# Performance work log

Hardware: AMD Instinct MI355X
Metric: run time of the kernel (lower is better)

Reference implementation:

```python
import jax, jax.numpy as jnp
import numpy as np
import math

N = 40000
E = 1280000
HID = 128
NF = 128
NG = 50
L = 3
CUTOFF = 10.0


def ssp(x):
    # shifted softplus: softplus(x) - log(2)
    return jax.nn.softplus(x) - jnp.float32(math.log(2.0))


def setup_inputs() -> dict:
    key = jax.random.key(0)
    ks = jax.random.split(key, 16)
    z = jax.random.randint(ks[0], (N,), 0, 100)
    pos = jax.random.normal(ks[1], (N, 3), dtype=jnp.float32) * 3.0
    batch = jnp.zeros((N,), dtype=jnp.int32)
    edge_index = jax.random.randint(ks[2], (2, E), 0, N)
    s = 0.1
    emb = jax.random.normal(ks[3], (100, HID), dtype=jnp.float32) * s
    mlp_w1 = jax.random.normal(ks[4], (L, NG, NF), dtype=jnp.float32) * s
    mlp_b1 = jnp.zeros((L, NF), dtype=jnp.float32)
    mlp_w2 = jax.random.normal(ks[5], (L, NF, NF), dtype=jnp.float32) * s
    mlp_b2 = jnp.zeros((L, NF), dtype=jnp.float32)
    conv_w1 = jax.random.normal(ks[6], (L, HID, NF), dtype=jnp.float32) * s  # no bias
    conv_w2 = jax.random.normal(ks[7], (L, NF, HID), dtype=jnp.float32) * s
    conv_b2 = jnp.zeros((L, HID), dtype=jnp.float32)
    lin_w = jax.random.normal(ks[8], (L, HID, HID), dtype=jnp.float32) * s
    lin_b = jnp.zeros((L, HID), dtype=jnp.float32)
    lin1_w = jax.random.normal(ks[9], (HID, HID // 2), dtype=jnp.float32) * s
    lin1_b = jnp.zeros((HID // 2,), dtype=jnp.float32)
    return {
        "z": z, "pos": pos, "batch": batch, "edge_index": edge_index,
        "emb": emb, "mlp_w1": mlp_w1, "mlp_b1": mlp_b1, "mlp_w2": mlp_w2,
        "mlp_b2": mlp_b2, "conv_w1": conv_w1, "conv_w2": conv_w2,
        "conv_b2": conv_b2, "lin_w": lin_w, "lin_b": lin_b,
        "lin1_w": lin1_w, "lin1_b": lin1_b,
    }


def reference(z, pos, batch, edge_index, emb, mlp_w1, mlp_b1, mlp_w2, mlp_b2,
              conv_w1, conv_w2, conv_b2, lin_w, lin_b, lin1_w, lin1_b):
    n = z.shape[0]
    row, col = edge_index[0], edge_index[1]
    # edge distances (radius-graph edge weights)
    diff = pos[row] - pos[col]                       # [E,3]
    edge_weight = jnp.sqrt(jnp.sum(diff * diff, axis=-1))  # [E]
    # Gaussian smearing
    offset = jnp.linspace(0.0, CUTOFF, NG, dtype=jnp.float32)
    coeff = -0.5 / (offset[1] - offset[0]) ** 2
    edge_attr = jnp.exp(coeff * (edge_weight[:, None] - offset[None, :]) ** 2)  # [E,NG]
    # cosine cutoff
    C = 0.5 * (jnp.cos(edge_weight * (jnp.pi / CUTOFF)) + 1.0)  # [E]

    h = emb[z]  # [N,HID]
    for l in range(L):
        W = ssp(edge_attr @ mlp_w1[l] + mlp_b1[l]) @ mlp_w2[l] + mlp_b2[l]  # [E,NF]
        W = W * C[:, None]
        x = h @ conv_w1[l]                      # [N,NF]
        msg = x[row] * W                        # gather + filter, [E,NF]
        agg = jax.ops.segment_sum(msg, col, num_segments=n)  # scatter-add, [N,NF]
        x = agg @ conv_w2[l] + conv_b2[l]       # [N,HID]
        x = ssp(x)
        x = x @ lin_w[l] + lin_b[l]
        h = h + x
    return ssp(h @ lin1_w + lin1_b)  # [N,HID//2]
```

## Files before the change

### kernel.cpp

```cpp
#include <hip/hip_runtime.h>
#include <math.h>


typedef _Float16 f16;
typedef _Float16 half8 __attribute__((ext_vector_type(8)));
typedef _Float16 half4v __attribute__((ext_vector_type(4)));
typedef float f32x4 __attribute__((ext_vector_type(4)));

#define NGAUSS 50
#define HIDF   128
#define NBINS  8192
#define DMAXF  40.0f
#define NLAYER 3
#define XST    132
#define BSHIFT 9
#define MAXBUCK 128
#define SCAP  20480

static __device__ __forceinline__ float sspf(float v) {
    return fmaxf(v, 0.0f) + log1pf(expf(-fabsf(v))) - 0.6931471805599453f;
}

__global__ __launch_bounds__(256) void k_stage(const int* __restrict__ ei,
                                               const float* __restrict__ pos,
                                               int* __restrict__ scnt,
                                               uint2* __restrict__ staging,
                                               int E, int nbuck) {
    const float SCALE = (float)(NBINS - 1) / DMAXF;
    __shared__ int bhist[MAXBUCK];
    __shared__ int boff[MAXBUCK];
    __shared__ int gpos[MAXBUCK];
    __shared__ uint2 recs[4096];
    __shared__ unsigned char lbuck[4096];
    int t = threadIdx.x;
    for (int i = t; i < nbuck; i += 256) bhist[i] = 0;
    __syncthreads();
    int e0 = blockIdx.x * 4096;
    int cnt_here = min(4096, E - e0);
    unsigned pay[16];
    unsigned short cc[16];
    short rk[16];
#pragma unroll
    for (int k = 0; k < 16; ++k) {
        int idx = t + k * 256;
        rk[k] = -1;
        if (idx < cnt_here) {
            int e = e0 + idx;
            int r = ei[e], c = ei[E + e];
            float dx = pos[3*r+0] - pos[3*c+0];
            float dy = pos[3*r+1] - pos[3*c+1];
            float dz = pos[3*r+2] - pos[3*c+2];
            float d = sqrtf(dx*dx + dy*dy + dz*dz);
            float u = fminf(d * SCALE, (float)(NBINS - 1));
            int i0 = min((int)u, NBINS - 2);
            float w0 = u - (float)i0;
            int wq = (int)(w0 * 8.0f + 0.5f);
            if (wq == 8) { i0 = min(i0 + 1, NBINS - 2); wq = 0; }
            pay[k] = ((unsigned)i0 << 19) | ((unsigned)wq << 16) | (unsigned)r;
            cc[k] = (unsigned short)c;
            rk[k] = (short)atomicAdd(&bhist[c >> BSHIFT], 1);
        }
    }
    __syncthreads();
    if (t == 0) {
        int run = 0;
        for (int b = 0; b < nbuck; ++b) { boff[b] = run; run += bhist[b]; }
    }
    __syncthreads();
    if (t < nbuck) gpos[t] = atomicAdd(&scnt[t], bhist[t]);
    __syncthreads();
#pragma unroll
    for (int k = 0; k < 16; ++k) {
        if (rk[k] >= 0) {
            int b = cc[k] >> BSHIFT;
            int slot = boff[b] + rk[k];
            recs[slot] = make_uint2(pay[k], (unsigned)cc[k]);
            lbuck[slot] = (unsigned char)b;
        }
    }
    __syncthreads();
    for (int i = t; i < cnt_here; i += 256) {
        int b = lbuck[i];
        staging[(size_t)b * SCAP + gpos[b] + (i - boff[b])] = recs[i];
    }
}

__global__ __launch_bounds__(1024) void k_place(const uint2* __restrict__ staging,
                                                const int* __restrict__ scnt,
                                                int* __restrict__ meta,
                                                int* __restrict__ offs,
                                                int n, int nbuck) {
    __shared__ int lcnt[512], loff[512], lcur[512];
    __shared__ int ldsm[SCAP];
    __shared__ int ebase_s;
    int b = blockIdx.x, t = threadIdx.x;
    int cntb = scnt[b];
    if (t == 0) {
        int run = 0;
        for (int j = 0; j < b; ++j) run += scnt[j];
        ebase_s = run;
    }
    for (int j = t; j < 512; j += 1024) { lcnt[j] = 0; lcur[j] = 0; }
    __syncthreads();
    int ebase = ebase_s;
    const uint2* sb = staging + (size_t)b * SCAP;
    for (int i = t; i < cntb; i += 1024)
        atomicAdd(&lcnt[sb[i].y & 511], 1);
    __syncthreads();
    if (t < 512) loff[t] = lcnt[t];
    __syncthreads();
    for (int o = 1; o < 512; o <<= 1) {
        int v = 0;
        if (t < 512) { v = loff[t]; if (t >= o) v += loff[t - o]; }
        __syncthreads();
        if (t < 512) loff[t] = v;
        __syncthreads();
    }
    int nb0 = b << BSHIFT;
    if (t < 512) {
        int node = nb0 + t;
        if (node < n) offs[node] = ebase + loff[t] - lcnt[t];
    }
    if (b == nbuck - 1 && t == 0) offs[n] = ebase + cntb;
    __syncthreads();
    for (int i = t; i < cntb; i += 1024) {
        uint2 r = sb[i];
        int cl = (int)(r.y & 511);
        int lpos = (loff[cl] - lcnt[cl]) + atomicAdd(&lcur[cl], 1);
        if (lpos < SCAP) ldsm[lpos] = (int)r.x;
        else meta[ebase + lpos] = (int)r.x;
    }
    __syncthreads();
    int lim = min(cntb, SCAP);
    for (int i = t; i < lim; i += 1024) meta[ebase + i] = ldsm[i];
}

__global__ __launch_bounds__(128) void k_table(const float* __restrict__ w1,
                                               const float* __restrict__ b1,
                                               const float* __restrict__ w2,
                                               const float* __restrict__ b2,
                                               f16* __restrict__ T) {
    const float DELTA = 10.0f / 49.0f;
    const float COEFF = -0.5f / (DELTA * DELTA);
    const float HSTEP = DMAXF / (float)(NBINS - 1);
    __shared__ float ea[8][NGAUSS];
    __shared__ float u[8][HIDF];
    int l = blockIdx.y, b0 = blockIdx.x * 8, j = threadIdx.x;
    for (int idx = j; idx < 8 * NGAUSS; idx += 128) {
        int bb = idx / NGAUSS, g = idx % NGAUSS;
        float d = (float)(b0 + bb) * HSTEP;
        float diff = d - (float)g * DELTA;
        ea[bb][g] = expf(COEFF * diff * diff);
    }
    __syncthreads();
    float acc[8];
    {
        float bias = b1[l * HIDF + j];
#pragma unroll
        for (int b = 0; b < 8; ++b) acc[b] = bias;
        const float* w1l = w1 + (size_t)l * NGAUSS * HIDF;
        for (int g = 0; g < NGAUSS; ++g) {
            float wv = w1l[g * HIDF + j];
#pragma unroll
            for (int b = 0; b < 8; ++b) acc[b] = fmaf(ea[b][g], wv, acc[b]);
        }
#pragma unroll
        for (int b = 0; b < 8; ++b) u[b][j] = sspf(acc[b]);
    }
    __syncthreads();
    {
        float bias = b2[l * HIDF + j];
#pragma unroll
        for (int b = 0; b < 8; ++b) acc[b] = bias;
        const float* w2l = w2 + (size_t)l * HIDF * HIDF;
        for (int k = 0; k < HIDF; ++k) {
            float wv = w2l[k * HIDF + j];
#pragma unroll
            for (int b = 0; b < 8; ++b) acc[b] = fmaf(u[b][k], wv, acc[b]);
        }
    }
    f16* Tl = T + ((size_t)l * NBINS + b0) * HIDF;
#pragma unroll
    for (int b = 0; b < 8; ++b) {
        float d = (float)(b0 + b) * HSTEP;
        float C = 0.5f * (cosf(d * (float)(M_PI / 10.0)) + 1.0f);
        Tl[b * HIDF + j] = (f16)(acc[b] * C);
    }
}

__global__ void k_wpack(const float* __restrict__ cw1, const float* __restrict__ cw2,
                        const float* __restrict__ lw, const float* __restrict__ l1w,
                        f16* __restrict__ Wp) {
    int mat = blockIdx.y;
    int N = (mat == 9) ? 64 : HIDF;
    int ntiles = N >> 4;
    int tid = blockIdx.x * 256 + threadIdx.x;
    int lane = tid & 63, ks = (tid >> 6) & 3, nt = tid >> 8;
    if (nt >= ntiles) return;
    const float* W;
    if (mat < 9) {
        int l = mat / 3, kind = mat % 3;
        W = (kind == 0 ? cw1 : kind == 1 ? cw2 : lw) + (size_t)l * HIDF * HIDF;
    } else {
        W = l1w;
    }
    int kbase = ks * 32 + (lane >> 4) * 8;
    int col = nt * 16 + (lane & 15);
    half8 st;
#pragma unroll
    for (int j = 0; j < 8; ++j) st[j] = (f16)W[(size_t)(kbase + j) * N + col];
    *(half8*)&Wp[(size_t)mat * 16384 + ((size_t)(nt * 4 + ks) * 64 + lane) * 8] = st;
}

#define AGG_EDGE(yy)                                                         \
    {                                                                        \
        int row_ = (yy) & 0xFFFF;                                            \
        int i0_ = ((unsigned)(yy)) >> 19;                                    \
        float w0_ = (float)(((yy) >> 16) & 7) * 0.125f;                      \
        half8 x0_ = *(const half8*)&xj[(size_t)row_ * HIDF];                 \
        half8 ta_ = *(const half8*)&Tj[(size_t)i0_ * HIDF];                  \
        half8 tb_ = *(const half8*)&Tj[(size_t)(i0_ + 1) * HIDF];            \
        _Pragma("unroll")                                                    \
        for (int j = 0; j < 8; ++j) {                                        \
            float t0 = (float)ta_[j];                                        \
            float f0 = fmaf(w0_, (float)tb_[j] - t0, t0);                    \
            a[j] = fmaf((float)x0_[j], f0, a[j]);                            \
        }                                                                    \
    }

__global__ __launch_bounds__(256) void k_agg(const f16* __restrict__ x,
                                             const f16* __restrict__ T,
                                             const int* __restrict__ meta,
                                             const int* __restrict__ offs,
                                             f16* __restrict__ agg, int n) {
    int node = (blockIdx.x * blockDim.x + threadIdx.x) >> 4;
    int lane = threadIdx.x & 15;
    if (node >= n) return;
    int beg = offs[node], end = offs[node + 1];
    const f16* xj = x + lane * 8;
    const f16* Tj = T + lane * 8;
    float a[8] = {};
    for (int chunk = beg; chunk < end; chunk += 16) {
        int cnt = min(16, end - chunk);
        int mm = meta[chunk + min(lane, cnt - 1)];
        int q = 0;
        for (; q + 4 <= cnt; q += 4) {
            int y0 = __shfl(mm, q + 0, 16);
            int y1 = __shfl(mm, q + 1, 16);
            int y2 = __shfl(mm, q + 2, 16);
            int y3 = __shfl(mm, q + 3, 16);
            AGG_EDGE(y0)
            AGG_EDGE(y1)
            AGG_EDGE(y2)
            AGG_EDGE(y3)
        }
        for (; q < cnt; ++q) {
            int y0 = __shfl(mm, q, 16);
            AGG_EDGE(y0)
        }
    }
    half8 st;
#pragma unroll
    for (int j = 0; j < 8; ++j) st[j] = (f16)a[j];
    *(half8*)&agg[(size_t)node * HIDF + lane * 8] = st;
}

__global__ __launch_bounds__(256) void k_init_gemm(const int* __restrict__ z,
                                                   const float* __restrict__ emb,
                                                   const f16* __restrict__ w1p,
                                                   f16* __restrict__ xout) {
    int lane = threadIdx.x & 63;
    int wid = threadIdx.x >> 6;
    int m0 = blockIdx.x * 64 + wid * 16;
    int mrow = lane & 15, quad = lane >> 4;
    const float* er = emb + (size_t)z[m0 + mrow] * HIDF + quad * 8;
    half8 afr[4];
#pragma unroll
    for (int ks = 0; ks < 4; ++ks) {
        float4 a = *(const float4*)(er + ks * 32);
        float4 b = *(const float4*)(er + ks * 32 + 4);
        half8 f = {(f16)a.x, (f16)a.y, (f16)a.z, (f16)a.w,
                   (f16)b.x, (f16)b.y, (f16)b.z, (f16)b.w};
        afr[ks] = f;
    }
    f32x4 acc[8];
#pragma unroll
    for (int t = 0; t < 8; ++t) acc[t] = (f32x4){0.f, 0.f, 0.f, 0.f};
    const f16* bp = w1p + (size_t)lane * 8;
#pragma unroll
    for (int t = 0; t < 8; ++t)
#pragma unroll
        for (int ks = 0; ks < 4; ++ks) {
            half8 bfr = *(const half8*)(bp + (size_t)(t * 4 + ks) * 512);
            acc[t] = __builtin_amdgcn_mfma_f32_16x16x32_f16(afr[ks], bfr, acc[t], 0, 0, 0);
        }
    int col0 = lane & 15;
    int growb = m0 + quad * 4;
#pragma unroll
    for (int t = 0; t < 8; ++t)
#pragma unroll
        for (int r = 0; r < 4; ++r)
            xout[(size_t)(growb + r) * HIDF + t * 16 + col0] = (f16)acc[t][r];
}

template <int NT3, bool LAYER0, bool WRITE_H>
__global__ __launch_bounds__(256) void k_fused(const f16* __restrict__ agg,
                                               const f16* __restrict__ w2p,
                                               const float* __restrict__ b2,
                                               const f16* __restrict__ lwp,
                                               const float* __restrict__ lb,
                                               const f16* __restrict__ b3p,
                                               const float* __restrict__ b3,
                                               float* __restrict__ hio,
                                               const int* __restrict__ z,
                                               const float* __restrict__ emb,
                                               f16* __restrict__ xout,
                                               float* __restrict__ fout) {
    __shared__ f16 Xs[4][16][XST];
    int lane = threadIdx.x & 63;
    int wid = threadIdx.x >> 6;
    int m0 = blockIdx.x * 64 + wid * 16;
    int mrow = lane & 15, quad = lane >> 4;
    int col0 = mrow;
    int growb = m0 + quad * 4;
    f16 (*X)[XST] = Xs[wid];

    half8 afr[4];
    {
        const f16* Ar = agg + (size_t)(m0 + mrow) * HIDF + quad * 8;
#pragma unroll
        for (int ks = 0; ks < 4; ++ks) afr[ks] = *(const half8*)(Ar + ks * 32);
    }
    f32x4 acc[8];
#pragma unroll
    for (int t = 0; t < 8; ++t) acc[t] = (f32x4){0.f, 0.f, 0.f, 0.f};
    {
        const f16* bp = w2p + (size_t)lane * 8;
#pragma unroll
        for (int t = 0; t < 8; ++t)
#pragma unroll
            for (int ks = 0; ks < 4; ++ks) {
                half8 bfr = *(const half8*)(bp + (size_t)(t * 4 + ks) * 512);
                acc[t] = __builtin_amdgcn_mfma_f32_16x16x32_f16(afr[ks], bfr, acc[t], 0, 0, 0);
            }
    }
#pragma unroll
    for (int t = 0; t < 8; ++t) {
        int col = t * 16 + col0;
        float bv = b2[col];
#pragma unroll
        for (int r = 0; r < 4; ++r)
            X[quad * 4 + r][col] = (f16)sspf(acc[t][r] + bv);
    }
#pragma unroll
    for (int ks = 0; ks < 4; ++ks) {
        half4v lo = *(const half4v*)&X[mrow][ks * 32 + quad * 8];
        half4v hi = *(const half4v*)&X[mrow][ks * 32 + quad * 8 + 4];
        half8 f;
#pragma unroll
        for (int j = 0; j < 4; ++j) { f[j] = lo[j]; f[4 + j] = hi[j]; }
        afr[ks] = f;
    }
#pragma unroll
    for (int t = 0; t < 8; ++t) acc[t] = (f32x4){0.f, 0.f, 0.f, 0.f};
    {
        const f16* bp = lwp + (size_t)lane * 8;
#pragma unroll
        for (int t = 0; t < 8; ++t)
#pragma unroll
            for (int ks = 0; ks < 4; ++ks) {
                half8 bfr = *(const half8*)(bp + (size_t)(t * 4 + ks) * 512);
                acc[t] = __builtin_amdgcn_mfma_f32_16x16x32_f16(afr[ks], bfr, acc[t], 0, 0, 0);
            }
    }
    int zr[4];
    if (LAYER0) {
#pragma unroll
        for (int r = 0; r < 4; ++r) zr[r] = z[growb + r];
    }
#pragma unroll
    for (int t = 0; t < 8; ++t) {
        int col = t * 16 + col0;
        float bv = lb[col];
#pragma unroll
        for (int r = 0; r < 4; ++r) {
            int grow = growb + r;
            float resid = LAYER0 ? emb[(size_t)zr[r] * HIDF + col]
                                 : hio[(size_t)grow * HIDF + col];
            float hp = acc[t][r] + bv + resid;
            if (WRITE_H) hio[(size_t)grow * HIDF + col] = hp;
            X[quad * 4 + r][col] = (f16)hp;
        }
    }
#pragma unroll
    for (int ks = 0; ks < 4; ++ks) {
        half4v lo = *(const half4v*)&X[mrow][ks * 32 + quad * 8];
        half4v hi = *(const half4v*)&X[mrow][ks * 32 + quad * 8 + 4];
        half8 f;
#pragma unroll
        for (int j = 0; j < 4; ++j) { f[j] = lo[j]; f[4 + j] = hi[j]; }
        afr[ks] = f;
    }
#pragma unroll
    for (int t = 0; t < NT3; ++t) acc[t] = (f32x4){0.f, 0.f, 0.f, 0.f};
    {
        const f16* bp = b3p + (size_t)lane * 8;
#pragma unroll
        for (int t = 0; t < NT3; ++t)
#pragma unroll
            for (int ks = 0; ks < 4; ++ks) {
                half8 bfr = *(const half8*)(bp + (size_t)(t * 4 + ks) * 512);
                acc[t] = __builtin_amdgcn_mfma_f32_16x16x32_f16(afr[ks], bfr, acc[t], 0, 0, 0);
            }
    }
    if (NT3 == 8) {
#pragma unroll
        for (int t = 0; t < 8; ++t)
#pragma unroll
            for (int r = 0; r < 4; ++r)
                xout[(size_t)(growb + r) * HIDF + t * 16 + col0] = (f16)acc[t][r];
    } else {
#pragma unroll
        for (int t = 0; t < NT3; ++t) {
            int col = t * 16 + col0;
            float bv = b3[col];
#pragma unroll
            for (int r = 0; r < 4; ++r)
                fout[(size_t)(growb + r) * (NT3 * 16) + col] = sspf(acc[t][r] + bv);
        }
    }
}

extern "C" void kernel_launch(void* const* d_in, const int* in_sizes, int n_in,
                              void* d_out, int out_size, void* d_ws, size_t ws_size,
                              hipStream_t stream) {
    const int*   z       = (const int*)d_in[0];
    const float* pos     = (const float*)d_in[1];
    const int*   ei      = (const int*)d_in[3];
    const float* emb     = (const float*)d_in[4];
    const float* mlp_w1  = (const float*)d_in[5];
    const float* mlp_b1  = (const float*)d_in[6];
    const float* mlp_w2  = (const float*)d_in[7];
    const float* mlp_b2  = (const float*)d_in[8];
    const float* conv_w1 = (const float*)d_in[9];
    const float* conv_w2 = (const float*)d_in[10];
    const float* conv_b2 = (const float*)d_in[11];
    const float* lin_w   = (const float*)d_in[12];
    const float* lin_b   = (const float*)d_in[13];
    const float* lin1_w  = (const float*)d_in[14];
    const float* lin1_b  = (const float*)d_in[15];
    float* out = (float*)d_out;

    int n = in_sizes[0];
    int E = in_sizes[3] / 2;
    int nbuck = (n + 511) >> 9;

    char* ws = (char*)d_ws;
    size_t off = 0;
    auto alloc = [&](size_t bytes) -> void* {
        void* p = ws + off;
        off = (off + bytes + 255) & ~(size_t)255;
        return p;
    };
    float* h     = (float*)alloc((size_t)n * HIDF * 4);
    f16*   x16   = (f16*)alloc((size_t)n * HIDF * 2);
    f16*   agg16 = (f16*)alloc((size_t)n * HIDF * 2);
    f16*   T16   = (f16*)alloc((size_t)NLAYER * NBINS * HIDF * 2);
    int*   meta  = (int*)alloc((size_t)E * 4);
    int*   offs  = (int*)alloc((size_t)(n + 1) * 4);
    int*   scnt  = (int*)alloc((size_t)nbuck * 4);
    uint2* staging = (uint2*)alloc((size_t)nbuck * SCAP * 8);
    f16*   Wp    = (f16*)alloc((size_t)10 * 16384 * 2);

    const int tb = 256;
    hipMemsetAsync(scnt, 0, (size_t)nbuck * 4, stream);
    hipLaunchKernelGGL(k_stage, dim3((E + 4095) / 4096), dim3(tb), 0, stream,
                       ei, pos, scnt, staging, E, nbuck);
    hipLaunchKernelGGL(k_place, dim3(nbuck), dim3(1024), 0, stream,
                       staging, scnt, meta, offs, n, nbuck);
    hipLaunchKernelGGL(k_wpack, dim3(8, 10), dim3(tb), 0, stream,
                       conv_w1, conv_w2, lin_w, lin1_w, Wp);
    hipLaunchKernelGGL(k_table, dim3(NBINS / 8, NLAYER), dim3(128), 0, stream,
                       mlp_w1, mlp_b1, mlp_w2, mlp_b2, T16);

    int gemmblocks = n / 64;
    int aggblocks = (n * 16 + tb - 1) / tb;
    hipLaunchKernelGGL(k_init_gemm, dim3(gemmblocks), dim3(tb), 0, stream,
                       z, emb, Wp + (size_t)0 * 16384, x16);
    hipLaunchKernelGGL(k_agg, dim3(aggblocks), dim3(tb), 0, stream,
                       x16, T16 + (size_t)0 * NBINS * HIDF, meta, offs, agg16, n);
    hipLaunchKernelGGL(HIP_KERNEL_NAME(k_fused<8, true, true>), dim3(gemmblocks), dim3(tb), 0, stream,
                       agg16, Wp + (size_t)1 * 16384, conv_b2 + 0 * HIDF,
                       Wp + (size_t)2 * 16384, lin_b + 0 * HIDF,
                       Wp + (size_t)3 * 16384, (const float*)nullptr,
                       h, z, emb, x16, (float*)nullptr);
    hipLaunchKernelGGL(k_agg, dim3(aggblocks), dim3(tb), 0, stream,
                       x16, T16 + (size_t)1 * NBINS * HIDF, meta, offs, agg16, n);
    hipLaunchKernelGGL(HIP_KERNEL_NAME(k_fused<8, false, true>), dim3(gemmblocks), dim3(tb), 0, stream,
                       agg16, Wp + (size_t)4 * 16384, conv_b2 + 1 * HIDF,
                       Wp + (size_t)5 * 16384, lin_b + 1 * HIDF,
                       Wp + (size_t)6 * 16384, (const float*)nullptr,
                       h, (const int*)nullptr, (const float*)nullptr, x16, (float*)nullptr);
    hipLaunchKernelGGL(k_agg, dim3(aggblocks), dim3(tb), 0, stream,
                       x16, T16 + (size_t)2 * NBINS * HIDF, meta, offs, agg16, n);
    hipLaunchKernelGGL(HIP_KERNEL_NAME(k_fused<4, false, false>), dim3(gemmblocks), dim3(tb), 0, stream,
                       agg16, Wp + (size_t)7 * 16384, conv_b2 + 2 * HIDF,
                       Wp + (size_t)8 * 16384, lin_b + 2 * HIDF,
                       Wp + (size_t)9 * 16384, lin1_b,
                       h, (const int*)nullptr, (const float*)nullptr, (f16*)nullptr, out);
    (void)n_in; (void)out_size; (void)ws_size;
}
```

Baseline: 436.8 us.

## Expand filter table to 64K bins and use nearest-bin lookup in aggregation

The coarse 8192-bin filter table is expanded by a new kernel into a fine 65536-bin table via linear interpolation, so each edge stores a single rounded bin index instead of a bin plus quantized weight. The aggregation loop drops the second table load and the interpolation math per edge, and is unrolled to issue eight edges' loads before the FMAs. The fine table is 48 MB across three layers, which may raise cache pressure, and the staging buffer is aliased onto the fine table memory. An extra expansion kernel is added to setup.

```diff
diff --git a/kernel.cpp b/kernel.cpp
--- a/kernel.cpp
+++ b/kernel.cpp
@@ -10,6 +10,7 @@
 #define NGAUSS 50
 #define HIDF   128
 #define NBINS  8192
+#define FBINS  65536
 #define DMAXF  40.0f
 #define NLAYER 3
 #define XST    132
@@ -26,7 +27,7 @@
                                                int* __restrict__ scnt,
                                                uint2* __restrict__ staging,
                                                int E, int nbuck) {
-    const float SCALE = (float)(NBINS - 1) / DMAXF;
+    const float SCALE = (float)(FBINS - 1) / DMAXF;
     __shared__ int bhist[MAXBUCK];
     __shared__ int boff[MAXBUCK];
     __shared__ int gpos[MAXBUCK];
@@ -51,12 +52,9 @@
             float dy = pos[3*r+1] - pos[3*c+1];
             float dz = pos[3*r+2] - pos[3*c+2];
             float d = sqrtf(dx*dx + dy*dy + dz*dz);
-            float u = fminf(d * SCALE, (float)(NBINS - 1));
-            int i0 = min((int)u, NBINS - 2);
-            float w0 = u - (float)i0;
-            int wq = (int)(w0 * 8.0f + 0.5f);
-            if (wq == 8) { i0 = min(i0 + 1, NBINS - 2); wq = 0; }
-            pay[k] = ((unsigned)i0 << 19) | ((unsigned)wq << 16) | (unsigned)r;
+            int ib = (int)(d * SCALE + 0.5f);
+            ib = min(ib, FBINS - 1);
+            pay[k] = ((unsigned)ib << 16) | (unsigned)r;
             cc[k] = (unsigned short)c;
             rk[k] = (short)atomicAdd(&bhist[c >> BSHIFT], 1);
         }
@@ -188,6 +186,25 @@
     }
 }
 
+__global__ __launch_bounds__(128) void k_expand(const f16* __restrict__ Tc,
+                                                f16* __restrict__ Tf) {
+    int l = blockIdx.y, j = threadIdx.x;
+    int fb0 = blockIdx.x * 16;
+    const f16* src = Tc + (size_t)l * NBINS * HIDF;
+    f16* dst = Tf + (size_t)l * FBINS * HIDF;
+    const float R = (float)(NBINS - 1) / (float)(FBINS - 1);
+#pragma unroll
+    for (int r = 0; r < 16; ++r) {
+        int fb = fb0 + r;
+        float u = (float)fb * R;
+        int i0 = min((int)u, NBINS - 2);
+        float w = u - (float)i0;
+        float c0 = (float)src[(size_t)i0 * HIDF + j];
+        float c1 = (float)src[(size_t)(i0 + 1) * HIDF + j];
+        dst[(size_t)fb * HIDF + j] = (f16)fmaf(w, c1 - c0, c0);
+    }
+}
+
 __global__ void k_wpack(const float* __restrict__ cw1, const float* __restrict__ cw2,
                         const float* __restrict__ lw, const float* __restrict__ l1w,
                         f16* __restrict__ Wp) {
@@ -211,22 +228,6 @@
     for (int j = 0; j < 8; ++j) st[j] = (f16)W[(size_t)(kbase + j) * N + col];
     *(half8*)&Wp[(size_t)mat * 16384 + ((size_t)(nt * 4 + ks) * 64 + lane) * 8] = st;
 }
-
-#define AGG_EDGE(yy)                                                         \
-    {                                                                        \
-        int row_ = (yy) & 0xFFFF;                                            \
-        int i0_ = ((unsigned)(yy)) >> 19;                                    \
-        float w0_ = (float)(((yy) >> 16) & 7) * 0.125f;                      \
-        half8 x0_ = *(const half8*)&xj[(size_t)row_ * HIDF];                 \
-        half8 ta_ = *(const half8*)&Tj[(size_t)i0_ * HIDF];                  \
-        half8 tb_ = *(const half8*)&Tj[(size_t)(i0_ + 1) * HIDF];            \
-        _Pragma("unroll")                                                    \
-        for (int j = 0; j < 8; ++j) {                                        \
-            float t0 = (float)ta_[j];                                        \
-            float f0 = fmaf(w0_, (float)tb_[j] - t0, t0);                    \
-            a[j] = fmaf((float)x0_[j], f0, a[j]);                            \
-        }                                                                    \
-    }
 
 __global__ __launch_bounds__(256) void k_agg(const f16* __restrict__ x,
                                              const f16* __restrict__ T,
@@ -244,19 +245,27 @@
         int cnt = min(16, end - chunk);
         int mm = meta[chunk + min(lane, cnt - 1)];
         int q = 0;
-        for (; q + 4 <= cnt; q += 4) {
-            int y0 = __shfl(mm, q + 0, 16);
-            int y1 = __shfl(mm, q + 1, 16);
-            int y2 = __shfl(mm, q + 2, 16);
-            int y3 = __shfl(mm, q + 3, 16);
-            AGG_EDGE(y0)
-            AGG_EDGE(y1)
-            AGG_EDGE(y2)
-            AGG_EDGE(y3)
+        for (; q + 8 <= cnt; q += 8) {
+            half8 xv[8], tv[8];
+#pragma unroll
+            for (int k = 0; k < 8; ++k) {
+                int y = __shfl(mm, q + k, 16);
+                xv[k] = *(const half8*)&xj[(size_t)(y & 0xFFFF) * HIDF];
+                tv[k] = *(const half8*)&Tj[(size_t)((unsigned)y >> 16) * HIDF];
+            }
+#pragma unroll
+            for (int k = 0; k < 8; ++k)
+#pragma unroll
+                for (int j = 0; j < 8; ++j)
+                    a[j] = fmaf((float)xv[k][j], (float)tv[k][j], a[j]);
         }
         for (; q < cnt; ++q) {
-            int y0 = __shfl(mm, q, 16);
-            AGG_EDGE(y0)
+            int y = __shfl(mm, q, 16);
+            half8 xv = *(const half8*)&xj[(size_t)(y & 0xFFFF) * HIDF];
+            half8 tv = *(const half8*)&Tj[(size_t)((unsigned)y >> 16) * HIDF];
+#pragma unroll
+            for (int j = 0; j < 8; ++j)
+                a[j] = fmaf((float)xv[j], (float)tv[j], a[j]);
         }
     }
     half8 st;
@@ -465,12 +474,13 @@
     float* h     = (float*)alloc((size_t)n * HIDF * 4);
     f16*   x16   = (f16*)alloc((size_t)n * HIDF * 2);
     f16*   agg16 = (f16*)alloc((size_t)n * HIDF * 2);
-    f16*   T16   = (f16*)alloc((size_t)NLAYER * NBINS * HIDF * 2);
+    f16*   Tc    = (f16*)alloc((size_t)NLAYER * NBINS * HIDF * 2);
+    f16*   Tf    = (f16*)alloc((size_t)NLAYER * FBINS * HIDF * 2);
     int*   meta  = (int*)alloc((size_t)E * 4);
     int*   offs  = (int*)alloc((size_t)(n + 1) * 4);
     int*   scnt  = (int*)alloc((size_t)nbuck * 4);
-    uint2* staging = (uint2*)alloc((size_t)nbuck * SCAP * 8);
     f16*   Wp    = (f16*)alloc((size_t)10 * 16384 * 2);
+    uint2* staging = (uint2*)Tf;
 
     const int tb = 256;
     hipMemsetAsync(scnt, 0, (size_t)nbuck * 4, stream);
@@ -478,31 +488,33 @@
                        ei, pos, scnt, staging, E, nbuck);
     hipLaunchKernelGGL(k_place, dim3(nbuck), dim3(1024), 0, stream,
                        staging, scnt, meta, offs, n, nbuck);
+    hipLaunchKernelGGL(k_table, dim3(NBINS / 8, NLAYER), dim3(128), 0, stream,
+                       mlp_w1, mlp_b1, mlp_w2, mlp_b2, Tc);
+    hipLaunchKernelGGL(k_expand, dim3(FBINS / 16, NLAYER), dim3(128), 0, stream,
+                       Tc, Tf);
     hipLaunchKernelGGL(k_wpack, dim3(8, 10), dim3(tb), 0, stream,
                        conv_w1, conv_w2, lin_w, lin1_w, Wp);
-    hipLaunchKernelGGL(k_table, dim3(NBINS / 8, NLAYER), dim3(128), 0, stream,
-                       mlp_w1, mlp_b1, mlp_w2, mlp_b2, T16);
 
     int gemmblocks = n / 64;
     int aggblocks = (n * 16 + tb - 1) / tb;
     hipLaunchKernelGGL(k_init_gemm, dim3(gemmblocks), dim3(tb), 0, stream,
                        z, emb, Wp + (size_t)0 * 16384, x16);
     hipLaunchKernelGGL(k_agg, dim3(aggblocks), dim3(tb), 0, stream,
-                       x16, T16 + (size_t)0 * NBINS * HIDF, meta, offs, agg16, n);
+                       x16, Tf + (size_t)0 * FBINS * HIDF, meta, offs, agg16, n);
     hipLaunchKernelGGL(HIP_KERNEL_NAME(k_fused<8, true, true>), dim3(gemmblocks), dim3(tb), 0, stream,
                        agg16, Wp + (size_t)1 * 16384, conv_b2 + 0 * HIDF,
                        Wp + (size_t)2 * 16384, lin_b + 0 * HIDF,
                        Wp + (size_t)3 * 16384, (const float*)nullptr,
                        h, z, emb, x16, (float*)nullptr);
     hipLaunchKernelGGL(k_agg, dim3(aggblocks), dim3(tb), 0, stream,
-                       x16, T16 + (size_t)1 * NBINS * HIDF, meta, offs, agg16, n);
+                       x16, Tf + (size_t)1 * FBINS * HIDF, meta, offs, agg16, n);
     hipLaunchKernelGGL(HIP_KERNEL_NAME(k_fused<8, false, true>), dim3(gemmblocks), dim3(tb), 0, stream,
                        agg16, Wp + (size_t)4 * 16384, conv_b2 + 1 * HIDF,
                        Wp + (size_t)5 * 16384, lin_b + 1 * HIDF,
                        Wp + (size_t)6 * 16384, (const float*)nullptr,
                        h, (const int*)nullptr, (const float*)nullptr, x16, (float*)nullptr);
     hipLaunchKernelGGL(k_agg, dim3(aggblocks), dim3(tb), 0, stream,
-                       x16, T16 + (size_t)2 * NBINS * HIDF, meta, offs, agg16, n);
+                       x16, Tf + (size_t)2 * FBINS * HIDF, meta, offs, agg16, n);
     hipLaunchKernelGGL(HIP_KERNEL_NAME(k_fused<4, false, false>), dim3(gemmblocks), dim3(tb), 0, stream,
                        agg16, Wp + (size_t)7 * 16384, conv_b2 + 2 * HIDF,
                        Wp + (size_t)8 * 16384, lin_b + 2 * HIDF,
```

Result: slower. 519.8 us (+19.0%).
